# Kernel tuning notes

Hardware: AMD Instinct MI355X
Metric: run time of the kernel (lower is better)

Reference implementation:

```python
import jax, jax.numpy as jnp
import numpy as np
from jax import lax

B = 4096          # graphs in batch
NPG = 50          # nodes per graph
N = B * NPG       # 204800 nodes
E = N * 8         # 1638400 directed edges
F_IN = 128
H = 64            # GCN hidden
K = 10            # SortPooling k
NUM_CLASSES = 10


def _glorot(key, shape):
    lim = float(np.sqrt(6.0 / (shape[0] + shape[1])))
    return jax.random.uniform(key, shape, jnp.float32, -lim, lim)


def setup_inputs() -> dict:
    key = jax.random.key(0)
    ks = jax.random.split(key, 10)
    x = jax.random.normal(ks[0], (N, F_IN), jnp.float32)
    edge_index = jax.random.randint(ks[1], (2, E), 0, N)
    batch = jnp.repeat(jnp.arange(B), NPG)  # sorted graph ids, 50 nodes each
    return {
        "x": x, "edge_index": edge_index, "batch": batch,
        "W1": _glorot(ks[2], (F_IN, H)), "b1": jnp.zeros((H,), jnp.float32),
        "W2": _glorot(ks[3], (H, H)), "b2": jnp.zeros((H,), jnp.float32),
        "W3": _glorot(ks[4], (H, H)), "b3": jnp.zeros((H,), jnp.float32),
        "Wc1": jax.random.normal(ks[5], (32, K, 4), jnp.float32) * 0.05,
        "bc1": jnp.zeros((32,), jnp.float32),
        "Wc2": jax.random.normal(ks[6], (64, 32, 3), jnp.float32) * 0.05,
        "bc2": jnp.zeros((64,), jnp.float32),
        "Wf": _glorot(ks[7], (H, NUM_CLASSES)),
        "bf": jnp.zeros((NUM_CLASSES,), jnp.float32),
    }


def reference(x, edge_index, batch, W1, b1, W2, b2, W3, b3, Wc1, bc1, Wc2, bc2, Wf, bf):
    row, col = edge_index[0], edge_index[1]
    # PyG GCNConv normalization with self-loops: deg over targets + 1
    deg = jax.ops.segment_sum(jnp.ones((E,), jnp.float32), col, num_segments=N) + 1.0
    dinv = lax.rsqrt(deg)
    ecoef = (dinv[row] * dinv[col])[:, None]   # [E,1] edge norm
    scoef = (dinv * dinv)[:, None]             # [N,1] self-loop norm

    def gcn(h, W, b):
        h = h @ W
        agg = jax.ops.segment_sum(h[row] * ecoef, col, num_segments=N) + h * scoef
        return agg + b

    x1 = jnp.tanh(gcn(x, W1, b1))
    x2 = jnp.tanh(gcn(x1, W2, b2))
    x3 = jnp.tanh(gcn(x2, W3, b3))
    feat = jnp.concatenate([x1, x2, x3], axis=-1)   # JK cat -> [N, 192]

    # DGL SortPooling(k=10): sort each node's features ascending, then take
    # top-k nodes per graph by the last (largest) feature, descending.
    feat = jnp.sort(feat, axis=-1)
    order = jnp.lexsort((-feat[:, -1], batch))      # graph asc, key desc
    fs, bs = feat[order], batch[order]
    counts = jax.ops.segment_sum(jnp.ones((N,), jnp.int32), batch, num_segments=B)
    starts = jnp.cumsum(counts) - counts
    rank = jnp.arange(N) - starts[bs]               # within-graph rank
    mask = (rank < K)[:, None]
    pooled = jnp.zeros((B, K, feat.shape[-1]), feat.dtype)
    pooled = pooled.at[bs, jnp.minimum(rank, K - 1)].add(jnp.where(mask, fs, 0.0))

    h = pooled  # [B, 10, 192] == x.view(B, 10, 192)
    h = lax.conv_general_dilated(h, Wc1, (4,), 'VALID',
                                 dimension_numbers=('NCH', 'OIH', 'NCH')) + bc1[None, :, None]
    h = jax.nn.relu(h)                              # [B,32,48]
    h = lax.reduce_window(h, -jnp.inf, lax.max, (1, 1, 4), (1, 1, 4), 'VALID')  # [B,32,12]
    h = lax.conv_general_dilated(h, Wc2, (3,), 'VALID',
                                 dimension_numbers=('NCH', 'OIH', 'NCH')) + bc2[None, :, None]
    h = jax.nn.relu(h)                              # [B,64,4]
    h = lax.reduce_window(h, -jnp.inf, lax.max, (1, 1, 4), (1, 1, 4), 'VALID')  # [B,64,1]
    xf = h.reshape(B, -1)                           # [B,64]
    c = jax.nn.relu(xf) @ Wf + bf                   # [B,num_classes]
    return (c, xf)
```

## Files before the change

kernel.cpp:

```cpp
#include <hip/hip_runtime.h>
#include <hip/hip_bf16.h>

#define NN 204800
#define EE 1638400
#define BBATCH 4096
#define NPGRAPH 50
#define KTOP 10
#define NBLK 200

#define OFF_W1  0
#define OFF_W2  8192
#define OFF_W3  12288
#define OFF_B1  16384
#define OFF_B2  16448
#define OFF_B3  16512
#define OFF_WC1 16576
#define OFF_BC1 17856
#define OFF_WC2 17888
#define OFF_BC2 24032
#define OFF_WF  24096
#define OFF_BF  24736
#define WTOT    24746

__device__ __forceinline__ float bf2f(unsigned short u) {
    unsigned int x = ((unsigned int)u) << 16;
    float f; __builtin_memcpy(&f, &x, 4); return f;
}

__device__ __forceinline__ long long pack_sc(int s, float c) {
    return ((long long)(unsigned)__float_as_int(c) << 32) | (unsigned)s;
}

__global__ void detect_kernel(const unsigned int* __restrict__ xw,
                              const unsigned int* __restrict__ eiw,
                              int* __restrict__ flags) {
    __shared__ int s_f32, s_i64;
    int t = threadIdx.x;
    if (t == 0) { s_f32 = 0; s_i64 = 1; }
    __syncthreads();
    unsigned w = xw[t];
    unsigned u0 = w & 0xffffu, u1 = w >> 16;
    int e0 = (u0 >> 7) & 0xff, e1 = (u1 >> 7) & 0xff;
    if (e0 >= 0x88 || e1 >= 0x88) atomicOr(&s_f32, 1);
    if (eiw[2 * t + 1] != 0) atomicAnd(&s_i64, 0);
    __syncthreads();
    if (t == 0) { flags[0] = s_f32; flags[1] = s_i64; }
}


struct WPtrs { const void* p[12]; };

__global__ void convert_weights_kernel(WPtrs wp, const int* __restrict__ flags,
                                       float* __restrict__ dst) {
    const int lens[12] = {8192,4096,4096,64,64,64,1280,32,6144,64,640,10};
    const int offs[12] = {OFF_W1,OFF_W2,OFF_W3,OFF_B1,OFF_B2,OFF_B3,
                          OFF_WC1,OFF_BC1,OFF_WC2,OFF_BC2,OFF_WF,OFF_BF};
    int f32 = flags[0];
    int t = blockIdx.x * 256 + threadIdx.x;
    for (int s = 0; s < 12; ++s) {
        if (t < lens[s]) {
            float v = f32 ? ((const float*)wp.p[s])[t]
                          : bf2f(((const unsigned short*)wp.p[s])[t]);
            dst[offs[s] + t] = v;
            return;
        }
        t -= lens[s];
    }
}


__global__ void zero_int_kernel(int* p, int n) {
    int i = blockIdx.x * 256 + threadIdx.x;
    if (i < n) p[i] = 0;
}

__device__ __forceinline__ int ld_idx(const void* ei, int i64, long pos) {
    return i64 ? (int)((const long long*)ei)[pos] : ((const int*)ei)[pos];
}

__global__ void count_kernel(const void* __restrict__ ei, const int* __restrict__ flags,
                             int* __restrict__ cnt) {
    int e = blockIdx.x * 256 + threadIdx.x;
    if (e >= EE) return;
    int c = ld_idx(ei, flags[1], (long)EE + e);
    atomicAdd(&cnt[c], 1);
}

__global__ __launch_bounds__(1024) void scan1_kernel(const int* __restrict__ cnt,
                                                     int* __restrict__ offs,
                                                     float* __restrict__ dinv,
                                                     int* __restrict__ blksum) {
    __shared__ int wsum[16];
    int b = blockIdx.x, t = threadIdx.x;
    int lane = t & 63, wid = t >> 6;
    int i = b * 1024 + t;
    int v = cnt[i] + 1;
    int x = v;
    #pragma unroll
    for (int d = 1; d < 64; d <<= 1) { int y = __shfl_up(x, d, 64); if (lane >= d) x += y; }
    if (lane == 63) wsum[wid] = x;
    __syncthreads();
    if (t == 0) {
        int run = 0;
        #pragma unroll
        for (int k = 0; k < 16; ++k) { int tmp = wsum[k]; wsum[k] = run; run += tmp; }
        blksum[b] = run;
    }
    __syncthreads();
    offs[i] = wsum[wid] + x - v;
    dinv[i] = (float)(1.0 / sqrt((double)v));
}

__global__ __launch_bounds__(256) void scan2_kernel(int* __restrict__ blksum) {
    __shared__ int wsum[4];
    int t = threadIdx.x, lane = t & 63, wid = t >> 6;
    int v = (t < NBLK) ? blksum[t] : 0;
    int x = v;
    #pragma unroll
    for (int d = 1; d < 64; d <<= 1) { int y = __shfl_up(x, d, 64); if (lane >= d) x += y; }
    if (lane == 63) wsum[wid] = x;
    __syncthreads();
    int pre = 0;
    for (int k = 0; k < wid; ++k) pre += wsum[k];
    if (t < NBLK) blksum[t] = pre + x - v;
}

__global__ __launch_bounds__(1024) void scan3_kernel(int* __restrict__ offs,
                                                     const int* __restrict__ blksum) {
    int b = blockIdx.x, i = b * 1024 + threadIdx.x;
    offs[i] += blksum[b];
    if (i == 0) offs[NN] = EE + NN;
}

__global__ void fill_self_kernel(const int* __restrict__ offs, const float* __restrict__ dinv,
                                 int* __restrict__ cursor, long long* __restrict__ epack) {
    int n = blockIdx.x * 256 + threadIdx.x;
    if (n >= NN) return;
    int p = offs[n];
    float d = dinv[n];
    __builtin_nontemporal_store(pack_sc(n, d * d), &epack[p]);
    cursor[n] = 1;
}

__global__ void fill_edges_kernel(const void* __restrict__ ei, const int* __restrict__ flags,
                                  const int* __restrict__ offs,
                                  const float* __restrict__ dinv, int* __restrict__ cursor,
                                  long long* __restrict__ epack) {
    int e = blockIdx.x * 256 + threadIdx.x;
    if (e >= EE) return;
    int i64 = flags[1];
    int r = ld_idx(ei, i64, e);
    int c = ld_idx(ei, i64, (long)EE + e);
    int p = offs[c] + atomicAdd(&cursor[c], 1);
    __builtin_nontemporal_store(pack_sc(r, dinv[r] * dinv[c]), &epack[p]);
}


template<int KD, int MODE>
__global__ __launch_bounds__(256) void xw_kernel(const void* __restrict__ xin_,
                                                 const int* __restrict__ flags,
                                                 int row_stride, int col_off,
                                                 const float* __restrict__ W,
                                                 float* __restrict__ hout) {
    constexpr int CH = 32;
    __shared__ float xs[256 * 36];
    int t = threadIdx.x;
    long row0 = (long)blockIdx.x * 256;
    bool bf16in = (MODE == 1) && (flags[0] == 0);
    float acc[64];
    #pragma unroll
    for (int c = 0; c < 64; ++c) acc[c] = 0.f;

    for (int kb = 0; kb < KD; kb += CH) {
        __syncthreads();
        if (bf16in) {
            const unsigned short* x = (const unsigned short*)xin_;
            unsigned short* xsh = (unsigned short*)xs;
            #pragma unroll
            for (int rr = 0; rr < 32; ++rr) {
                int idx = rr * 256 + t;
                int r = idx >> 5, k = idx & 31;
                xsh[r * 40 + k] = x[(row0 + r) * row_stride + col_off + kb + k];
            }
        } else {
            const float* x = (const float*)xin_;
            #pragma unroll
            for (int rr = 0; rr < 32; ++rr) {
                int idx = rr * 256 + t;
                int r = idx >> 5, k = idx & 31;
                xs[r * 36 + k] = x[(row0 + r) * row_stride + col_off + kb + k];
            }
        }
        __syncthreads();
        if (bf16in) {
            #pragma unroll 2
            for (int k = 0; k < CH; ++k) {
                float xk = bf2f(((unsigned short*)xs)[t * 40 + k]);
                const float* wr = W + (kb + k) * 64;
                #pragma unroll
                for (int c = 0; c < 64; ++c) acc[c] = fmaf(xk, wr[c], acc[c]);
            }
        } else {
            #pragma unroll 2
            for (int k = 0; k < CH; ++k) {
                float xk = xs[t * 36 + k];
                const float* wr = W + (kb + k) * 64;
                #pragma unroll
                for (int c = 0; c < 64; ++c) acc[c] = fmaf(xk, wr[c], acc[c]);
            }
        }
    }
    float* o = hout + (row0 + t) * 64;
    #pragma unroll
    for (int c = 0; c < 64; c += 4) {
        float4 v; v.x = acc[c]; v.y = acc[c+1]; v.z = acc[c+2]; v.w = acc[c+3];
        *(float4*)(o + c) = v;
    }
}


__global__ __launch_bounds__(256) void spmm_kernel(const float* __restrict__ h,
                                                   const int* __restrict__ offs,
                                                   const long long* __restrict__ epack,
                                                   const float* __restrict__ bias,
                                                   float* __restrict__ featOut,
                                                   float* __restrict__ keyOut) {
    int node = blockIdx.x * 4 + (threadIdx.x >> 6);
    int lane = threadIdx.x & 63;
    int j0 = offs[node], j1 = offs[node + 1];
    float acc = 0.f;

    for (int base = j0; base < j1; base += 64) {
        int n = j1 - base; if (n > 64) n = 64;
        long long my = 0;
        if (lane < n) my = epack[base + lane];

        int m = 0;
        for (; m + 8 <= n; m += 8) {
            float hv[8], cf[8];
            #pragma unroll
            for (int u = 0; u < 8; ++u) {
                long long e = __shfl(my, m + u, 64);
                int s = (int)(unsigned)e;
                cf[u] = __int_as_float((int)(e >> 32));
                hv[u] = h[(long)s * 64 + lane];
            }
            #pragma unroll
            for (int u = 0; u < 8; ++u) acc = fmaf(hv[u], cf[u], acc);
        }
        for (; m < n; ++m) {
            long long e = __shfl(my, m, 64);
            int s = (int)(unsigned)e;
            float cf = __int_as_float((int)(e >> 32));
            acc = fmaf(h[(long)s * 64 + lane], cf, acc);
        }
    }

    float val = tanhf(acc + bias[lane]);
    featOut[(long)node * 192 + lane] = val;
    float m = val;
    #pragma unroll
    for (int d = 32; d; d >>= 1) m = fmaxf(m, __shfl_xor(m, d, 64));
    if (lane == 0) keyOut[node] = m;
}


__global__ __launch_bounds__(256) void select_topk_kernel(const float* __restrict__ key3,
                                                          int* __restrict__ topidx) {
    int g = blockIdx.x * 4 + (threadIdx.x >> 6);
    int lane = threadIdx.x & 63;
    int node = g * NPGRAPH + lane;
    float k = -INFINITY;
    if (lane < NPGRAPH)
        k = fmaxf(fmaxf(key3[node], key3[NN + node]), key3[2 * NN + node]);
    for (int r = 0; r < KTOP; ++r) {
        float bk = k; int bi = lane;
        #pragma unroll
        for (int d = 32; d; d >>= 1) {
            float ok = __shfl_xor(bk, d, 64);
            int   oi = __shfl_xor(bi, d, 64);
            if (ok > bk || (ok == bk && oi < bi)) { bk = ok; bi = oi; }
        }
        if (lane == 0) topidx[g * KTOP + r] = g * NPGRAPH + bi;
        if (lane == bi) k = -INFINITY;
    }
}


__global__ __launch_bounds__(256) void sort_gather_kernel(const float* __restrict__ feat,
                                                          const int* __restrict__ topidx,
                                                          float* __restrict__ pooled) {
    int lane = threadIdx.x & 63;
    int w = threadIdx.x >> 6;
    int slot = blockIdx.x * 4 + w;
    int node = topidx[slot];

    unsigned v[4];
    #pragma unroll
    for (int t = 0; t < 3; ++t) {
        float x = feat[(long)node * 192 + 64 * t + lane];
        unsigned u = __float_as_uint(x);
        v[t] = (u & 0x80000000u) ? ~u : (u | 0x80000000u);
    }
    v[3] = 0xFF800000u;

    #pragma unroll
    for (int k = 2; k <= 256; k <<= 1) {
        #pragma unroll
        for (int d = 128; d >= 1; d >>= 1) {
            if (d >= k) continue;
            if (d >= 64) {
                int dt = d >> 6;
                #pragma unroll
                for (int t = 0; t < 4; ++t) {
                    if (!(t & dt)) {
                        int t2 = t | dt;
                        bool asc = ((64 * t) & k) == 0;
                        unsigned a = v[t], b = v[t2];
                        unsigned mn = a < b ? a : b;
                        unsigned mx = a < b ? b : a;
                        v[t]  = asc ? mn : mx;
                        v[t2] = asc ? mx : mn;
                    }
                }
            } else {
                #pragma unroll
                for (int t = 0; t < 4; ++t) {
                    unsigned p = (unsigned)__shfl_xor((int)v[t], d, 64);
                    int e = 64 * t + lane;
                    bool lower = (lane & d) == 0;
                    bool asc = (e & k) == 0;
                    unsigned mn = v[t] < p ? v[t] : p;
                    unsigned mx = v[t] < p ? p : v[t];
                    v[t] = (lower == asc) ? mn : mx;
                }
            }
        }
    }

    #pragma unroll
    for (int t = 0; t < 3; ++t) {
        unsigned kk = v[t];
        unsigned u = (kk & 0x80000000u) ? (kk ^ 0x80000000u) : ~kk;
        pooled[(long)slot * 192 + 64 * t + lane] = __uint_as_float(u);
    }
}


__global__ __launch_bounds__(256) void conv1_kernel(const float* __restrict__ pooled,
                                                    const float* __restrict__ wc,
                                                    float* __restrict__ pool1) {
    __shared__ float p[1920];
    __shared__ float w[1280];
    __shared__ float c1[1536];
    int b = blockIdx.x, t = threadIdx.x;
    for (int i = t; i < 1920; i += 256) p[i] = pooled[(long)b * 1920 + i];
    for (int i = t; i < 1280; i += 256) w[i] = wc[OFF_WC1 + i];
    __syncthreads();
    for (int o = t; o < 1536; o += 256) {
        int oc = o / 48, s = o % 48;
        float acc = wc[OFF_BC1 + oc];
        #pragma unroll
        for (int ic = 0; ic < 10; ++ic)
            #pragma unroll
            for (int t4 = 0; t4 < 4; ++t4)
                acc = fmaf(p[ic * 192 + s * 4 + t4], w[oc * 40 + ic * 4 + t4], acc);
        c1[o] = fmaxf(acc, 0.f);
    }
    __syncthreads();
    for (int o = t; o < 384; o += 256) {
        int oc = o / 12, q = o % 12;
        float m = c1[oc * 48 + q * 4];
        #pragma unroll
        for (int u = 1; u < 4; ++u) m = fmaxf(m, c1[oc * 48 + q * 4 + u]);
        pool1[(long)b * 384 + o] = m;
    }
}


__global__ __launch_bounds__(256) void conv2_fc_kernel(const float* __restrict__ pool1,
                                                       const float* __restrict__ wc,
                                                       const int* __restrict__ flags,
                                                       void* __restrict__ outv) {
    __shared__ float p[384];
    __shared__ float w2[6144];
    __shared__ float r2[256];
    __shared__ float xfs[64];
    int b = blockIdx.x, t = threadIdx.x;
    int f32o = flags[0];
    for (int i = t; i < 384; i += 256) p[i] = pool1[(long)b * 384 + i];
    for (int i = t; i < 6144; i += 256) w2[i] = wc[OFF_WC2 + i];
    __syncthreads();
    {
        int oc = t >> 2, s = t & 3;
        float acc = wc[OFF_BC2 + oc];
        #pragma unroll
        for (int ic = 0; ic < 32; ++ic)
            #pragma unroll
            for (int t3 = 0; t3 < 3; ++t3)
                acc = fmaf(p[ic * 12 + 3 * s + t3], w2[oc * 96 + ic * 3 + t3], acc);
        r2[t] = fmaxf(acc, 0.f);
    }
    __syncthreads();
    if (t < 64) {
        float m = fmaxf(fmaxf(r2[4*t], r2[4*t+1]), fmaxf(r2[4*t+2], r2[4*t+3]));
        xfs[t] = m;
        long idx = (long)BBATCH * 10 + (long)b * 64 + t;
        if (f32o) ((float*)outv)[idx] = m;
        else      ((__hip_bfloat16*)outv)[idx] = __float2bfloat16(m);
    }
    __syncthreads();
    if (t < 10) {
        float acc = wc[OFF_BF + t];
        #pragma unroll
        for (int o = 0; o < 64; ++o)
            acc = fmaf(fmaxf(xfs[o], 0.f), wc[OFF_WF + o * 10 + t], acc);
        long idx = (long)b * 10 + t;
        if (f32o) ((float*)outv)[idx] = acc;
        else      ((__hip_bfloat16*)outv)[idx] = __float2bfloat16(acc);
    }
}


extern "C" void kernel_launch(void* const* d_in, const int* in_sizes, int n_in,
                              void* d_out, int out_size, void* d_ws, size_t ws_size,
                              hipStream_t stream) {
    const void* x  = d_in[0];
    const void* ei = d_in[1];
    WPtrs wp;
    wp.p[0] = d_in[3];
    wp.p[1] = d_in[5];
    wp.p[2] = d_in[7];
    wp.p[3] = d_in[4];
    wp.p[4] = d_in[6];
    wp.p[5] = d_in[8];
    wp.p[6] = d_in[9];
    wp.p[7] = d_in[10];
    wp.p[8] = d_in[11];
    wp.p[9] = d_in[12];
    wp.p[10] = d_in[13];
    wp.p[11] = d_in[14];

    char* ws = (char*)d_ws;
    size_t o = 0;
    auto take = [&](size_t bytes) { char* r = ws + o; o = (o + bytes + 255) & ~(size_t)255; return r; };
    int*       flags  = (int*)      take(2 * 4);
    float*     wconv  = (float*)    take((size_t)WTOT * 4);
    int*       offs   = (int*)      take((size_t)(NN + 1) * 4);
    long long* epack  = (long long*)take((size_t)(EE + NN) * 8);
    float*     key3   = (float*)    take((size_t)3 * NN * 4);
    int*       topidx = (int*)      take((size_t)BBATCH * KTOP * 4);
    int*       blksum = (int*)      take((size_t)NBLK * 4);
    char*      hbase  = take((size_t)NN * 64 * 4);
    float*     feat   = (float*)    take((size_t)NN * 192 * 4);

    float* h      = (float*)hbase;
    int*   cnt    = (int*)(hbase);
    int*   cursor = (int*)(hbase + (1u << 20));
    float* dinv   = (float*)(hbase + (2u << 20));
    float* pooled = (float*)(hbase);
    float* pool1  = (float*)(hbase + (34u << 20));

    detect_kernel<<<1, 256, 0, stream>>>((const unsigned int*)x, (const unsigned int*)ei, flags);
    convert_weights_kernel<<<(WTOT + 255) / 256, 256, 0, stream>>>(wp, flags, wconv);
    zero_int_kernel<<<NN / 256, 256, 0, stream>>>(cnt, NN);
    count_kernel<<<EE / 256, 256, 0, stream>>>(ei, flags, cnt);
    scan1_kernel<<<NBLK, 1024, 0, stream>>>(cnt, offs, dinv, blksum);
    scan2_kernel<<<1, 256, 0, stream>>>(blksum);
    scan3_kernel<<<NBLK, 1024, 0, stream>>>(offs, blksum);
    fill_self_kernel<<<NN / 256, 256, 0, stream>>>(offs, dinv, cursor, epack);
    fill_edges_kernel<<<EE / 256, 256, 0, stream>>>(ei, flags, offs, dinv, cursor, epack);

    xw_kernel<128, 1><<<NN / 256, 256, 0, stream>>>(x, flags, 128, 0, wconv + OFF_W1, h);
    spmm_kernel<<<NN / 4, 256, 0, stream>>>(h, offs, epack, wconv + OFF_B1, feat, key3);
    xw_kernel<64, 0><<<NN / 256, 256, 0, stream>>>(feat, flags, 192, 0, wconv + OFF_W2, h);
    spmm_kernel<<<NN / 4, 256, 0, stream>>>(h, offs, epack, wconv + OFF_B2, feat + 64, key3 + NN);
    xw_kernel<64, 0><<<NN / 256, 256, 0, stream>>>(feat, flags, 192, 64, wconv + OFF_W3, h);
    spmm_kernel<<<NN / 4, 256, 0, stream>>>(h, offs, epack, wconv + OFF_B3, feat + 128, key3 + 2 * NN);

    select_topk_kernel<<<BBATCH / 4, 256, 0, stream>>>(key3, topidx);
    sort_gather_kernel<<<BBATCH * KTOP / 4, 256, 0, stream>>>(feat, topidx, pooled);
    conv1_kernel<<<BBATCH, 256, 0, stream>>>(pooled, wconv, pool1);
    conv2_fc_kernel<<<BBATCH, 256, 0, stream>>>(pool1, wconv, flags, d_out);
}
```

Before: 978.8 us.

## Use bf16 MFMA for the dense XW products when inputs are bf16

Adds an MFMA-based XW kernel that runs when the inputs are bf16, using pre-transposed bf16 weights prepared by a small new kernel. Layer one feeds the bf16 x straight into 16x16x32 MFMAs. Layers two and three split the fp32 activations into hi and lo bf16 parts so accuracy stays close to fp32. The old scalar LDS kernel now returns early on the bf16 path and stays as the fp32 fallback. This costs one extra launch per layer plus the weight-prep kernel. Rounding the weights to bf16 loses some precision.

Measured after the change: 1.075 ms. 9.9% more time.

```diff
diff --git a/kernel.cpp b/kernel.cpp
--- a/kernel.cpp
+++ b/kernel.cpp
@@ -22,6 +22,9 @@
 #define OFF_BF  24736
 #define WTOT    24746
 
+typedef __bf16 bf16x8 __attribute__((ext_vector_type(8)));
+typedef float  f32x4  __attribute__((ext_vector_type(4)));
+
 __device__ __forceinline__ float bf2f(unsigned short u) {
     unsigned int x = ((unsigned int)u) << 16;
     float f; __builtin_memcpy(&f, &x, 4); return f;
@@ -68,6 +71,21 @@
     }
 }
 
+__global__ void prep_wt_kernel(const float* __restrict__ wconv,
+                               __bf16* __restrict__ wt) {
+    int i = blockIdx.x * 256 + threadIdx.x;
+    if (i < 8192) {
+        int c = i >> 7, k = i & 127;
+        wt[i] = (__bf16)wconv[OFF_W1 + k * 64 + c];
+    } else if (i < 12288) {
+        int j = i - 8192; int c = j >> 6, k = j & 63;
+        wt[i] = (__bf16)wconv[OFF_W2 + k * 64 + c];
+    } else if (i < 16384) {
+        int j = i - 12288; int c = j >> 6, k = j & 63;
+        wt[i] = (__bf16)wconv[OFF_W3 + k * 64 + c];
+    }
+}
+
 
 __global__ void zero_int_kernel(int* p, int n) {
     int i = blockIdx.x * 256 + threadIdx.x;
@@ -156,12 +174,90 @@
 }
 
 
+template<int MODE>
+__global__ __launch_bounds__(256) void xw_mfma_kernel(const void* __restrict__ A_,
+                                                      const int* __restrict__ flags,
+                                                      int row_stride, int col_off,
+                                                      const __bf16* __restrict__ Wt,
+                                                      float* __restrict__ hout) {
+    if (flags[0] != 0) return;
+    constexpr int KW = (MODE == 1) ? 128 : 64;
+    const int L = threadIdx.x & 63;
+    const int w = threadIdx.x >> 6;
+    const int rsub = L & 15;
+    const int ko = (L >> 4) * 8;
+
+    bf16x8 bfrag[4][KW / 32];
+    #pragma unroll
+    for (int ct = 0; ct < 4; ++ct)
+        #pragma unroll
+        for (int kb = 0; kb < KW / 32; ++kb)
+            bfrag[ct][kb] = *reinterpret_cast<const bf16x8*>(
+                Wt + (ct * 16 + rsub) * KW + kb * 32 + ko);
+
+    #pragma unroll 1
+    for (int it = 0; it < 4; ++it) {
+        long row0 = ((long)blockIdx.x * 4 + it) * 64 + w * 16;
+        long r = row0 + rsub;
+        f32x4 acc[4] = {{0.f,0.f,0.f,0.f},{0.f,0.f,0.f,0.f},
+                        {0.f,0.f,0.f,0.f},{0.f,0.f,0.f,0.f}};
+
+        if (MODE == 1) {
+            const __bf16* ap = (const __bf16*)A_ + r * 128;
+            bf16x8 afr[4];
+            #pragma unroll
+            for (int kb = 0; kb < 4; ++kb)
+                afr[kb] = *reinterpret_cast<const bf16x8*>(ap + kb * 32 + ko);
+            #pragma unroll
+            for (int kb = 0; kb < 4; ++kb)
+                #pragma unroll
+                for (int ct = 0; ct < 4; ++ct)
+                    acc[ct] = __builtin_amdgcn_mfma_f32_16x16x32_bf16(
+                        afr[kb], bfrag[ct][kb], acc[ct], 0, 0, 0);
+        } else {
+            const float* ap = (const float*)A_ + r * row_stride + col_off;
+            f32x4 v[2][2];
+            #pragma unroll
+            for (int kb = 0; kb < 2; ++kb) {
+                v[kb][0] = *reinterpret_cast<const f32x4*>(ap + kb * 32 + ko);
+                v[kb][1] = *reinterpret_cast<const f32x4*>(ap + kb * 32 + ko + 4);
+            }
+            #pragma unroll
+            for (int kb = 0; kb < 2; ++kb) {
+                bf16x8 ah, al;
+                #pragma unroll
+                for (int e = 0; e < 8; ++e) {
+                    float x = v[kb][e >> 2][e & 3];
+                    __bf16 hi = (__bf16)x;
+                    ah[e] = hi;
+                    al[e] = (__bf16)(x - (float)hi);
+                }
+                #pragma unroll
+                for (int ct = 0; ct < 4; ++ct) {
+                    acc[ct] = __builtin_amdgcn_mfma_f32_16x16x32_bf16(
+                        ah, bfrag[ct][kb], acc[ct], 0, 0, 0);
+                    acc[ct] = __builtin_amdgcn_mfma_f32_16x16x32_bf16(
+                        al, bfrag[ct][kb], acc[ct], 0, 0, 0);
+                }
+            }
+        }
+        float* hp = hout + row0 * 64;
+        #pragma unroll
+        for (int ct = 0; ct < 4; ++ct)
+            #pragma unroll
+            for (int j = 0; j < 4; ++j)
+                hp[((L >> 4) * 4 + j) * 64 + ct * 16 + rsub] = acc[ct][j];
+    }
+}
+
+
 template<int KD, int MODE>
 __global__ __launch_bounds__(256) void xw_kernel(const void* __restrict__ xin_,
                                                  const int* __restrict__ flags,
                                                  int row_stride, int col_off,
                                                  const float* __restrict__ W,
                                                  float* __restrict__ hout) {
+    if (flags[0] == 0) return;
     constexpr int CH = 32;
     __shared__ float xs[256 * 36];
     int t = threadIdx.x;
@@ -446,6 +542,7 @@
     auto take = [&](size_t bytes) { char* r = ws + o; o = (o + bytes + 255) & ~(size_t)255; return r; };
     int*       flags  = (int*)      take(2 * 4);
     float*     wconv  = (float*)    take((size_t)WTOT * 4);
+    __bf16*    wt     = (__bf16*)   take((size_t)16384 * 2);
     int*       offs   = (int*)      take((size_t)(NN + 1) * 4);
     long long* epack  = (long long*)take((size_t)(EE + NN) * 8);
     float*     key3   = (float*)    take((size_t)3 * NN * 4);
@@ -463,6 +560,7 @@
 
     detect_kernel<<<1, 256, 0, stream>>>((const unsigned int*)x, (const unsigned int*)ei, flags);
     convert_weights_kernel<<<(WTOT + 255) / 256, 256, 0, stream>>>(wp, flags, wconv);
+    prep_wt_kernel<<<64, 256, 0, stream>>>(wconv, wt);
     zero_int_kernel<<<NN / 256, 256, 0, stream>>>(cnt, NN);
     count_kernel<<<EE / 256, 256, 0, stream>>>(ei, flags, cnt);
     scan1_kernel<<<NBLK, 1024, 0, stream>>>(cnt, offs, dinv, blksum);
@@ -471,10 +569,13 @@
     fill_self_kernel<<<NN / 256, 256, 0, stream>>>(offs, dinv, cursor, epack);
     fill_edges_kernel<<<EE / 256, 256, 0, stream>>>(ei, flags, offs, dinv, cursor, epack);
 
+    xw_mfma_kernel<1><<<800, 256, 0, stream>>>(x, flags, 128, 0, wt, h);
     xw_kernel<128, 1><<<NN / 256, 256, 0, stream>>>(x, flags, 128, 0, wconv + OFF_W1, h);
     spmm_kernel<<<NN / 4, 256, 0, stream>>>(h, offs, epack, wconv + OFF_B1, feat, key3);
+    xw_mfma_kernel<0><<<800, 256, 0, stream>>>(feat, flags, 192, 0, wt + 8192, h);
     xw_kernel<64, 0><<<NN / 256, 256, 0, stream>>>(feat, flags, 192, 0, wconv + OFF_W2, h);
     spmm_kernel<<<NN / 4, 256, 0, stream>>>(h, offs, epack, wconv + OFF_B2, feat + 64, key3 + NN);
+    xw_mfma_kernel<0><<<800, 256, 0, stream>>>(feat, flags, 192, 64, wt + 12288, h);
     xw_kernel<64, 0><<<NN / 256, 256, 0, stream>>>(feat, flags, 192, 64, wconv + OFF_W3, h);
     spmm_kernel<<<NN / 4, 256, 0, stream>>>(h, offs, epack, wconv + OFF_B3, feat + 128, key3 + 2 * NN);
 
```

## Split XW output columns across thread halves and double-buffer fp32 input tiles

Applied to the files above, without the earlier changes.

The dense X·W kernel now handles 128 rows per block, with each thread computing 32 output columns instead of 64. This halves accumulator registers and doubles the grid size, aiming for better occupancy. The fp32 path loads input with float4 register prefetch of the next K chunk into a double-buffered shared tile, overlapping global loads with FMAs. Each weight row is now read by twice as many threads overall, and the fp32 path uses a padded stride of 33.

Result: faster. 879.4 us (-10.2%).

```diff
diff --git a/kernel.cpp b/kernel.cpp
--- a/kernel.cpp
+++ b/kernel.cpp
@@ -162,57 +162,82 @@
                                                  int row_stride, int col_off,
                                                  const float* __restrict__ W,
                                                  float* __restrict__ hout) {
-    constexpr int CH = 32;
-    __shared__ float xs[256 * 36];
-    int t = threadIdx.x;
-    long row0 = (long)blockIdx.x * 256;
-    bool bf16in = (MODE == 1) && (flags[0] == 0);
-    float acc[64];
-    #pragma unroll
-    for (int c = 0; c < 64; ++c) acc[c] = 0.f;
-
-    for (int kb = 0; kb < KD; kb += CH) {
-        __syncthreads();
-        if (bf16in) {
-            const unsigned short* x = (const unsigned short*)xin_;
-            unsigned short* xsh = (unsigned short*)xs;
+    __shared__ float xs[2][128 * 33];
+    const int t = threadIdx.x;
+    const int row = t & 127;
+    const int cgs = __builtin_amdgcn_readfirstlane(t >> 7);
+    const long row0 = (long)blockIdx.x * 128;
+    const bool bf16in = (MODE == 1) && (flags[0] == 0);
+
+    float acc[32];
+    #pragma unroll
+    for (int c = 0; c < 32; ++c) acc[c] = 0.f;
+
+    if (bf16in) {
+        const unsigned short* xg = (const unsigned short*)xin_;
+        unsigned short* xsh = (unsigned short*)&xs[0][0];
+        for (int kb = 0; kb < KD; kb += 32) {
+            __syncthreads();
             #pragma unroll
-            for (int rr = 0; rr < 32; ++rr) {
-                int idx = rr * 256 + t;
+            for (int u = 0; u < 16; ++u) {
+                int idx = u * 256 + t;
                 int r = idx >> 5, k = idx & 31;
-                xsh[r * 40 + k] = x[(row0 + r) * row_stride + col_off + kb + k];
-            }
-        } else {
-            const float* x = (const float*)xin_;
+                xsh[r * 66 + k] = xg[(row0 + r) * row_stride + col_off + kb + k];
+            }
+            __syncthreads();
+            const unsigned short* xrow = xsh + row * 66;
+            const float* wb = W + (long)kb * 64 + cgs * 32;
+            #pragma unroll 2
+            for (int k = 0; k < 32; ++k) {
+                float xk = bf2f(xrow[k]);
+                const float* wr = wb + (long)k * 64;
+                #pragma unroll
+                for (int c = 0; c < 32; ++c) acc[c] = fmaf(xk, wr[c], acc[c]);
+            }
+        }
+    } else {
+        const float* xg = (const float*)xin_;
+        float4 rg[4];
+        #pragma unroll
+        for (int u = 0; u < 4; ++u) {
+            int f4 = u * 256 + t;
+            int r = f4 >> 3, k4 = f4 & 7;
+            rg[u] = *(const float4*)(xg + (row0 + r) * row_stride + col_off + k4 * 4);
+        }
+        int cur = 0;
+        for (int kb = 0; kb < KD; kb += 32) {
             #pragma unroll
-            for (int rr = 0; rr < 32; ++rr) {
-                int idx = rr * 256 + t;
-                int r = idx >> 5, k = idx & 31;
-                xs[r * 36 + k] = x[(row0 + r) * row_stride + col_off + kb + k];
-            }
-        }
-        __syncthreads();
-        if (bf16in) {
+            for (int u = 0; u < 4; ++u) {
+                int f4 = u * 256 + t;
+                int r = f4 >> 3, k4 = f4 & 7;
+                float* d = &xs[cur][r * 33 + k4 * 4];
+                d[0] = rg[u].x; d[1] = rg[u].y; d[2] = rg[u].z; d[3] = rg[u].w;
+            }
+            if (kb + 32 < KD) {
+                #pragma unroll
+                for (int u = 0; u < 4; ++u) {
+                    int f4 = u * 256 + t;
+                    int r = f4 >> 3, k4 = f4 & 7;
+                    rg[u] = *(const float4*)(xg + (row0 + r) * row_stride + col_off + kb + 32 + k4 * 4);
+                }
+            }
+            __syncthreads();
+            const float* xrow = &xs[cur][row * 33];
+            const float* wb = W + (long)kb * 64 + cgs * 32;
             #pragma unroll 2
-            for (int k = 0; k < CH; ++k) {
-                float xk = bf2f(((unsigned short*)xs)[t * 40 + k]);
-                const float* wr = W + (kb + k) * 64;
+            for (int k = 0; k < 32; ++k) {
+                float xk = xrow[k];
+                const float* wr = wb + (long)k * 64;
                 #pragma unroll
-                for (int c = 0; c < 64; ++c) acc[c] = fmaf(xk, wr[c], acc[c]);
-            }
-        } else {
-            #pragma unroll 2
-            for (int k = 0; k < CH; ++k) {
-                float xk = xs[t * 36 + k];
-                const float* wr = W + (kb + k) * 64;
-                #pragma unroll
-                for (int c = 0; c < 64; ++c) acc[c] = fmaf(xk, wr[c], acc[c]);
-            }
-        }
-    }
-    float* o = hout + (row0 + t) * 64;
-    #pragma unroll
-    for (int c = 0; c < 64; c += 4) {
+                for (int c = 0; c < 32; ++c) acc[c] = fmaf(xk, wr[c], acc[c]);
+            }
+            cur ^= 1;
+        }
+    }
+
+    float* o = hout + (row0 + row) * 64 + cgs * 32;
+    #pragma unroll
+    for (int c = 0; c < 32; c += 4) {
         float4 v; v.x = acc[c]; v.y = acc[c+1]; v.z = acc[c+2]; v.w = acc[c+3];
         *(float4*)(o + c) = v;
     }
@@ -471,11 +496,11 @@
     fill_self_kernel<<<NN / 256, 256, 0, stream>>>(offs, dinv, cursor, epack);
     fill_edges_kernel<<<EE / 256, 256, 0, stream>>>(ei, flags, offs, dinv, cursor, epack);
 
-    xw_kernel<128, 1><<<NN / 256, 256, 0, stream>>>(x, flags, 128, 0, wconv + OFF_W1, h);
+    xw_kernel<128, 1><<<NN / 128, 256, 0, stream>>>(x, flags, 128, 0, wconv + OFF_W1, h);
     spmm_kernel<<<NN / 4, 256, 0, stream>>>(h, offs, epack, wconv + OFF_B1, feat, key3);
-    xw_kernel<64, 0><<<NN / 256, 256, 0, stream>>>(feat, flags, 192, 0, wconv + OFF_W2, h);
+    xw_kernel<64, 0><<<NN / 128, 256, 0, stream>>>(feat, flags, 192, 0, wconv + OFF_W2, h);
     spmm_kernel<<<NN / 4, 256, 0, stream>>>(h, offs, epack, wconv + OFF_B2, feat + 64, key3 + NN);
-    xw_kernel<64, 0><<<NN / 256, 256, 0, stream>>>(feat, flags, 192, 64, wconv + OFF_W3, h);
+    xw_kernel<64, 0><<<NN / 128, 256, 0, stream>>>(feat, flags, 192, 64, wconv + OFF_W3, h);
     spmm_kernel<<<NN / 4, 256, 0, stream>>>(h, offs, epack, wconv + OFF_B3, feat + 128, key3 + 2 * NN);
 
     select_topk_kernel<<<BBATCH / 4, 256, 0, stream>>>(key3, topidx);
```
